# Kernel tuning notes

Measured on AMD Instinct MI355X. Metric: run time of the kernel, lower is better.

The kernel has to match this reference:

```python
import jax, jax.numpy as jnp
import numpy as np
from functools import partial

L, B, E, H, NL = 512, 16, 768, 12, 12
D = E // H  # head dim = 64
FF = 4 * E
LN_EPS = 1e-5


def gelu_new(x):
    # HF openai-gpt ACT_FNS['gelu'] (tanh approximation)
    c = np.sqrt(2.0 / np.pi).astype(np.float32)
    return 0.5 * x * (1.0 + jnp.tanh(c * (x + 0.044715 * x * x * x)))


def layer_norm(x, g, b):
    mu = jnp.mean(x, axis=-1, keepdims=True)
    var = jnp.mean(jnp.square(x - mu), axis=-1, keepdims=True)
    return (x - mu) * jax.lax.rsqrt(var + LN_EPS) * g + b


def setup_inputs() -> dict:
    key = jax.random.key(0)
    ks = jax.random.split(key, 8)
    s = 0.02
    x = jax.random.normal(ks[0], (L, B, E), dtype=jnp.float32)
    custom_mask = jnp.ones((B, L), dtype=jnp.float32)
    pos_emb = s * jax.random.normal(ks[1], (L, E), dtype=jnp.float32)
    # stacked per-layer params (leading axis = layer)
    params = {
        'c_attn_w': s * jax.random.normal(ks[2], (NL, E, 3 * E), dtype=jnp.float32),
        'c_attn_b': jnp.zeros((NL, 3 * E), dtype=jnp.float32),
        'attn_proj_w': s * jax.random.normal(ks[3], (NL, E, E), dtype=jnp.float32),
        'attn_proj_b': jnp.zeros((NL, E), dtype=jnp.float32),
        'ln1_g': jnp.ones((NL, E), dtype=jnp.float32),
        'ln1_b': jnp.zeros((NL, E), dtype=jnp.float32),
        'c_fc_w': s * jax.random.normal(ks[4], (NL, E, FF), dtype=jnp.float32),
        'c_fc_b': jnp.zeros((NL, FF), dtype=jnp.float32),
        'mlp_proj_w': s * jax.random.normal(ks[5], (NL, FF, E), dtype=jnp.float32),
        'mlp_proj_b': jnp.zeros((NL, E), dtype=jnp.float32),
        'ln2_g': jnp.ones((NL, E), dtype=jnp.float32),
        'ln2_b': jnp.zeros((NL, E), dtype=jnp.float32),
    }
    return {'x': x, 'custom_mask': custom_mask, 'pos_emb': pos_emb, **params}


def _gpt_forward(x, custom_mask, pos_emb, c_attn_w, c_attn_b, attn_proj_w,
                 attn_proj_b, ln1_g, ln1_b, c_fc_w, c_fc_b, mlp_proj_w,
                 mlp_proj_b, ln2_g, ln2_b):
    Lx, Bx, Ex = x.shape
    h = x.transpose(1, 0, 2) + pos_emb[None, :Lx]  # (B, L, E); dropout = eval identity
    # additive padding mask: (1 - m) * finfo.min, broadcast over heads/queries
    add_mask = (1.0 - custom_mask)[:, None, None, :] * jnp.finfo(jnp.float32).min
    causal = jnp.tril(jnp.ones((Lx, Lx), dtype=jnp.float32))  # bias buffer b

    def block(h, p):
        (caw, cab, apw, apb, g1, b1, fw, fb, pw, pb, g2, b2) = p
        qkv = h @ caw + cab                              # (B, L, 3E)
        q, k, v = jnp.split(qkv, 3, axis=-1)
        q = q.reshape(Bx, Lx, H, D).transpose(0, 2, 1, 3)  # (B, H, L, D)
        k = k.reshape(Bx, Lx, H, D).transpose(0, 2, 1, 3)
        v = v.reshape(Bx, Lx, H, D).transpose(0, 2, 1, 3)
        w = jnp.einsum('bhqd,bhkd->bhqk', q, k) / np.float32(np.sqrt(D))
        w = w * causal + (-10000.0) * (1.0 - causal)     # causal bias masking
        w = w + add_mask
        a = jax.nn.softmax(w, axis=-1)
        o = jnp.einsum('bhqk,bhkd->bhqd', a, v)          # (B, H, L, D)
        o = o.transpose(0, 2, 1, 3).reshape(Bx, Lx, Ex)
        a_out = o @ apw + apb
        n = layer_norm(h + a_out, g1, b1)
        m = gelu_new(n @ fw + fb) @ pw + pb
        h2 = layer_norm(n + m, g2, b2)
        return h2, None

    params = (c_attn_w, c_attn_b, attn_proj_w, attn_proj_b, ln1_g, ln1_b,
              c_fc_w, c_fc_b, mlp_proj_w, mlp_proj_b, ln2_g, ln2_b)
    h, _ = jax.lax.scan(block, h, params)
    return h.transpose(1, 0, 2)  # back to (L, B, E)


def reference(x, custom_mask, pos_emb, c_attn_w, c_attn_b, attn_proj_w,
              attn_proj_b, ln1_g, ln1_b, c_fc_w, c_fc_b, mlp_proj_w,
              mlp_proj_b, ln2_g, ln2_b):
    return _gpt_forward(x, custom_mask, pos_emb, c_attn_w, c_attn_b,
                        attn_proj_w, attn_proj_b, ln1_g, ln1_b, c_fc_w,
                        c_fc_b, mlp_proj_w, mlp_proj_b, ln2_g, ln2_b)
```

## Files before the change

kernel.cpp:

```cpp
#include <hip/hip_runtime.h>
#include <cstdint>
#include <cstddef>


#define LSEQ 512
#define NBATCH 16
#define EDIM 768
#define NHEAD 12
#define NLAYER 12

typedef __attribute__((ext_vector_type(8))) short short8;
typedef __attribute__((ext_vector_type(4))) float f32x4;

__device__ __forceinline__ short f2bf(float f) {
  union { float f; unsigned u; } x; x.f = f;
  return (short)((x.u + 0x7FFFu + ((x.u >> 16) & 1u)) >> 16);
}

__device__ __forceinline__ void gload_lds16(const void* g, void* l) {
  __builtin_amdgcn_global_load_lds(
      (__attribute__((address_space(1))) void*)(void*)g,
      (__attribute__((address_space(3))) void*)l, 16, 0, 0);
}

__global__ __launch_bounds__(256) void wt_transpose(const float* __restrict__ W,
                                                    short* __restrict__ Wt,
                                                    int K, int N) {
  __shared__ float tile[32][33];
  const int n0 = blockIdx.x * 32, k0 = blockIdx.y * 32;
  const size_t lo = (size_t)blockIdx.z * K * N;
  const float* Ws = W + lo;
  short* Wd = Wt + lo;
  const int tx = threadIdx.x & 31, ty = threadIdx.x >> 5;
#pragma unroll
  for (int i = 0; i < 4; ++i)
    tile[ty + i * 8][tx] = Ws[(size_t)(k0 + ty + i * 8) * N + n0 + tx];
  __syncthreads();
#pragma unroll
  for (int i = 0; i < 4; ++i)
    Wd[(size_t)(n0 + ty + i * 8) * K + k0 + tx] = f2bf(tile[tx][ty + i * 8]);
}

__global__ __launch_bounds__(256) void embed_k(const float* __restrict__ x,
                                               const float* __restrict__ pos,
                                               float* __restrict__ h,
                                               short* __restrict__ hbf) {
  const int row = blockIdx.x;
  const int b = row >> 9, lp = row & 511;
  const int t = threadIdx.x;
#pragma unroll
  for (int i = 0; i < 3; ++i) {
    const int e = t + i * 256;
    float v = x[(size_t)(lp * 16 + b) * 768 + e] + pos[(size_t)lp * 768 + e];
    h[(size_t)row * 768 + e] = v;
    hbf[(size_t)row * 768 + e] = f2bf(v);
  }
}

__global__ __launch_bounds__(256) void final_k(const float* __restrict__ h,
                                               float* __restrict__ out) {
  const int row = blockIdx.x;
  const int lp = row >> 4, b = row & 15;
  const int t = threadIdx.x;
#pragma unroll
  for (int i = 0; i < 3; ++i) {
    const int e = t + i * 256;
    out[(size_t)row * 768 + e] = h[(size_t)(b * 512 + lp) * 768 + e];
  }
}

__global__ __launch_bounds__(256) void ln_fused(const float* __restrict__ A,
                                                const float* __restrict__ B,
                                                const float* __restrict__ g,
                                                const float* __restrict__ be,
                                                float* __restrict__ outf,
                                                short* __restrict__ outb) {
  const int row = blockIdx.x;
  const int t = threadIdx.x;
  const size_t base = (size_t)row * 768;
  float v[3];
  float s1 = 0.f, s2 = 0.f;
#pragma unroll
  for (int i = 0; i < 3; ++i) {
    const int e = t + i * 256;
    float xv = A[base + e] + B[base + e];
    v[i] = xv; s1 += xv; s2 += xv * xv;
  }
#pragma unroll
  for (int m = 1; m < 64; m <<= 1) {
    s1 += __shfl_xor(s1, m);
    s2 += __shfl_xor(s2, m);
  }
  __shared__ float r1[4], r2[4];
  const int w = t >> 6, l = t & 63;
  if (l == 0) { r1[w] = s1; r2[w] = s2; }
  __syncthreads();
  s1 = r1[0] + r1[1] + r1[2] + r1[3];
  s2 = r2[0] + r2[1] + r2[2] + r2[3];
  const float mu = s1 * (1.f / 768.f);
  const float var = s2 * (1.f / 768.f) - mu * mu;
  const float rs = rsqrtf(var + 1e-5f);
#pragma unroll
  for (int i = 0; i < 3; ++i) {
    const int e = t + i * 256;
    float o = (v[i] - mu) * rs * g[e] + be[e];
    outf[base + e] = o;
    outb[base + e] = f2bf(o);
  }
}

template <int TN, int EPI>
__global__ __launch_bounds__(256) void gemm_bt(const short* __restrict__ A,
                                               const short* __restrict__ Bt,
                                               const float* __restrict__ bias,
                                               void* __restrict__ C,
                                               int N, int K) {
  constexpr int BK = 64;
  __shared__ alignas(16) short Alds[128 * BK];
  __shared__ alignas(16) short Blds[TN * BK];
  const int t = threadIdx.x;
  const int w = t >> 6, l = t & 63;
  constexpr int WR = (TN == 128) ? 2 : 4;
  constexpr int WC = (TN == 128) ? 2 : 1;
  constexpr int WM = 128 / WR;
  constexpr int MI = WM / 16;
  constexpr int NI = (TN / WC) / 16;
  const int wr = (WC == 2) ? (w >> 1) : w;
  const int wc = (WC == 2) ? (w & 1) : 0;
  const int l15 = l & 15, lhi = l >> 4;
  const int rowA0 = blockIdx.x * 128;
  const int rowB0 = blockIdx.y * TN;
  f32x4 acc[MI][NI];
#pragma unroll
  for (int mi = 0; mi < MI; ++mi)
#pragma unroll
    for (int ni = 0; ni < NI; ++ni) acc[mi][ni] = (f32x4){0.f, 0.f, 0.f, 0.f};

  const int srl = l >> 3;
  const int ss = l & 7;

  for (int kt = 0; kt < K; kt += BK) {
#pragma unroll
    for (int i = 0; i < 4; ++i) {
      const int r = i * 32 + w * 8 + srl;
      gload_lds16(A + (size_t)(rowA0 + r) * K + kt + ((ss ^ (r & 7)) << 3),
                  &Alds[i * 2048 + w * 512]);
    }
#pragma unroll
    for (int i = 0; i < TN / 32; ++i) {
      const int r = i * 32 + w * 8 + srl;
      gload_lds16(Bt + (size_t)(rowB0 + r) * K + kt + ((ss ^ (r & 7)) << 3),
                  &Blds[i * 2048 + w * 512]);
    }
    __syncthreads();
    short8 af[MI][2], bfr[NI][2];
#pragma unroll
    for (int mi = 0; mi < MI; ++mi) {
      const int r = wr * WM + mi * 16 + l15;
#pragma unroll
      for (int kc = 0; kc < 2; ++kc)
        af[mi][kc] = *(const short8*)
            &Alds[r * 64 + ((((kc << 2) | lhi) ^ (r & 7)) << 3)];
    }
#pragma unroll
    for (int ni = 0; ni < NI; ++ni) {
      const int r = wc * 64 + ni * 16 + l15;
#pragma unroll
      for (int kc = 0; kc < 2; ++kc)
        bfr[ni][kc] = *(const short8*)
            &Blds[r * 64 + ((((kc << 2) | lhi) ^ (r & 7)) << 3)];
    }
#pragma unroll
    for (int mi = 0; mi < MI; ++mi)
#pragma unroll
      for (int ni = 0; ni < NI; ++ni)
#pragma unroll
        for (int kc = 0; kc < 2; ++kc)
          acc[mi][ni] = __builtin_amdgcn_mfma_f32_16x16x32_bf16(
              af[mi][kc], bfr[ni][kc], acc[mi][ni], 0, 0, 0);
    __syncthreads();
  }

  float bv[NI];
#pragma unroll
  for (int ni = 0; ni < NI; ++ni) bv[ni] = bias[rowB0 + wc * 64 + ni * 16 + l15];
#pragma unroll
  for (int mi = 0; mi < MI; ++mi) {
#pragma unroll
    for (int ni = 0; ni < NI; ++ni) {
      const int col = rowB0 + wc * 64 + ni * 16 + l15;
#pragma unroll
      for (int i = 0; i < 4; ++i) {
        const int row = rowA0 + wr * WM + mi * 16 + lhi * 4 + i;
        float v = acc[mi][ni][i] + bv[ni];
        if constexpr (EPI == 0) {
          ((float*)C)[(size_t)row * N + col] = v;
        } else if constexpr (EPI == 1) {
          ((short*)C)[(size_t)row * N + col] = f2bf(v);
        } else {
          float z = 0.7978845608028654f * (v + 0.044715f * v * v * v);
          float th = 1.0f - 2.0f / (__expf(2.0f * z) + 1.0f);
          ((short*)C)[(size_t)row * N + col] = f2bf(0.5f * v * (1.0f + th));
        }
      }
    }
  }
}

__global__ __launch_bounds__(256) void attn_k(const short* __restrict__ qkv,
                                              const float* __restrict__ mask,
                                              short* __restrict__ o) {
  const int qb = blockIdx.x;
  const int hh = blockIdx.y;
  const int b = blockIdx.z;
  const int t = threadIdx.x, w = t >> 6, l = t & 63;
  const int l15 = l & 15, lhi = l >> 4;
  __shared__ alignas(16) short Klds[64 * 64];
  __shared__ alignas(16) short Vlds[64 * 64];
  __shared__ alignas(16) short Plds[4][16 * 72];

  short8 qa[2];
  {
    const size_t base =
        (size_t)(b * LSEQ + qb * 64 + w * 16 + l15) * 2304 + hh * 64;
    qa[0] = *(const short8*)&qkv[base + lhi * 8];
    qa[1] = *(const short8*)&qkv[base + 32 + lhi * 8];
  }
  float mrow[4] = {-1e30f, -1e30f, -1e30f, -1e30f};
  float lrow[4] = {0.f, 0.f, 0.f, 0.f};
  const f32x4 zero4 = {0.f, 0.f, 0.f, 0.f};
  f32x4 oacc[4];
#pragma unroll
  for (int nt = 0; nt < 4; ++nt) oacc[nt] = zero4;

  const int nkt = qb + 1;
  for (int kt = 0; kt < nkt; ++kt) {
    __syncthreads();
    {
      const int kr = t >> 2, cc = (t & 3) * 16;
      const size_t grow = (size_t)(b * LSEQ + kt * 64 + kr) * 2304 + hh * 64;
      short8 k0 = *(const short8*)&qkv[grow + 768 + cc];
      short8 k1 = *(const short8*)&qkv[grow + 768 + cc + 8];
      short8 v0 = *(const short8*)&qkv[grow + 1536 + cc];
      short8 v1 = *(const short8*)&qkv[grow + 1536 + cc + 8];
      const int sw = (kr & 7) << 4;
      *(short8*)((char*)Klds + ((kr * 128 + cc * 2) ^ sw)) = k0;
      *(short8*)((char*)Klds + ((kr * 128 + cc * 2 + 16) ^ sw)) = k1;
#pragma unroll
      for (int e = 0; e < 8; ++e) {
        const int n0 = cc + e, n1 = cc + 8 + e;
        ((short*)Vlds)[((n0 * 128 + kr * 2) ^ ((n0 & 7) << 4)) >> 1] = v0[e];
        ((short*)Vlds)[((n1 * 128 + kr * 2) ^ ((n1 & 7) << 4)) >> 1] = v1[e];
      }
    }
    __syncthreads();

    f32x4 s[4];
#pragma unroll
    for (int jt = 0; jt < 4; ++jt) {
      f32x4 z = zero4;
#pragma unroll
      for (int kc = 0; kc < 2; ++kc) {
        const int rowk = jt * 16 + l15;
        short8 kb = *(const short8*)((char*)Klds +
                     ((rowk * 128 + kc * 64 + lhi * 16) ^ ((rowk & 7) << 4)));
        z = __builtin_amdgcn_mfma_f32_16x16x32_bf16(qa[kc], kb, z, 0, 0, 0);
      }
      s[jt] = z;
    }

    float addm[4];
#pragma unroll
    for (int jt = 0; jt < 4; ++jt)
      addm[jt] = (1.0f - mask[b * LSEQ + kt * 64 + jt * 16 + l15]) *
                 -3.402823466e38f;
#pragma unroll
    for (int jt = 0; jt < 4; ++jt) {
      const int colg = kt * 64 + jt * 16 + l15;
#pragma unroll
      for (int i = 0; i < 4; ++i) {
        const int rowg = qb * 64 + w * 16 + lhi * 4 + i;
        float sv = s[jt][i] * 0.125f;
        if (colg > rowg) sv = -10000.0f;
        s[jt][i] = sv + addm[jt];
      }
    }

    float mnew[4], sc[4];
#pragma unroll
    for (int i = 0; i < 4; ++i) {
      float tm = fmaxf(fmaxf(s[0][i], s[1][i]), fmaxf(s[2][i], s[3][i]));
#pragma unroll
      for (int mm = 1; mm < 16; mm <<= 1) tm = fmaxf(tm, __shfl_xor(tm, mm));
      mnew[i] = fmaxf(mrow[i], tm);
      sc[i] = __expf(mrow[i] - mnew[i]);
      mrow[i] = mnew[i];
    }
#pragma unroll
    for (int i = 0; i < 4; ++i) {
      float ts = 0.f;
#pragma unroll
      for (int jt = 0; jt < 4; ++jt) {
        float p = __expf(s[jt][i] - mnew[i]);
        s[jt][i] = p;
        ts += p;
      }
#pragma unroll
      for (int mm = 1; mm < 16; mm <<= 1) ts += __shfl_xor(ts, mm);
      lrow[i] = lrow[i] * sc[i] + ts;
      oacc[0][i] *= sc[i]; oacc[1][i] *= sc[i];
      oacc[2][i] *= sc[i]; oacc[3][i] *= sc[i];
    }

    short* Pw = &Plds[w][0];
#pragma unroll
    for (int jt = 0; jt < 4; ++jt)
#pragma unroll
      for (int i = 0; i < 4; ++i)
        Pw[(lhi * 4 + i) * 72 + jt * 16 + l15] = f2bf(s[jt][i]);
    __syncthreads();
    short8 pa[2];
#pragma unroll
    for (int kc = 0; kc < 2; ++kc)
      pa[kc] = *(const short8*)&Pw[l15 * 72 + kc * 32 + lhi * 8];

#pragma unroll
    for (int nt = 0; nt < 4; ++nt) {
#pragma unroll
      for (int kc = 0; kc < 2; ++kc) {
        const int rown = nt * 16 + l15;
        short8 vb = *(const short8*)((char*)Vlds +
                     ((rown * 128 + kc * 64 + lhi * 16) ^ ((rown & 7) << 4)));
        oacc[nt] = __builtin_amdgcn_mfma_f32_16x16x32_bf16(pa[kc], vb,
                                                           oacc[nt], 0, 0, 0);
      }
    }
  }

#pragma unroll
  for (int i = 0; i < 4; ++i) {
    const size_t row = (size_t)(b * LSEQ + qb * 64 + w * 16 + lhi * 4 + i);
    const float inv = 1.0f / lrow[i];
#pragma unroll
    for (int nt = 0; nt < 4; ++nt)
      o[row * 768 + hh * 64 + nt * 16 + l15] = f2bf(oacc[nt][i] * inv);
  }
}

extern "C" void kernel_launch(void* const* d_in, const int* in_sizes, int n_in,
                              void* d_out, int out_size, void* d_ws,
                              size_t ws_size, hipStream_t stream) {
  const float* x    = (const float*)d_in[0];
  const float* mask = (const float*)d_in[1];
  const float* pos  = (const float*)d_in[2];
  const float* caw  = (const float*)d_in[3];
  const float* cab  = (const float*)d_in[4];
  const float* apw  = (const float*)d_in[5];
  const float* apb  = (const float*)d_in[6];
  const float* g1   = (const float*)d_in[7];
  const float* b1   = (const float*)d_in[8];
  const float* fw   = (const float*)d_in[9];
  const float* fb   = (const float*)d_in[10];
  const float* pw   = (const float*)d_in[11];
  const float* pb   = (const float*)d_in[12];
  const float* g2   = (const float*)d_in[13];
  const float* b2   = (const float*)d_in[14];

  char* ws = (char*)d_ws;
  size_t off = 0;
  auto alloc = [&](size_t bytes) {
    size_t o = off;
    off += (bytes + 255) & ~(size_t)255;
    return o;
  };
  float* h    = (float*)(ws + alloc(8192ull * 768 * 4));
  short* hbf  = (short*)(ws + alloc(8192ull * 768 * 2));
  float* nrm  = (float*)(ws + alloc(8192ull * 768 * 4));
  short* nbf  = (short*)(ws + alloc(8192ull * 768 * 2));
  short* qkvb = (short*)(ws + alloc(8192ull * 2304 * 2));
  short* obf  = (short*)(ws + alloc(8192ull * 768 * 2));
  float* aout = (float*)(ws + alloc(8192ull * 768 * 4));
  short* gbf  = (short*)(ws + alloc(8192ull * 3072 * 2));
  short* wt_attn = (short*)(ws + alloc(12ull * 768 * 2304 * 2));
  short* wt_proj = (short*)(ws + alloc(12ull * 768 * 768 * 2));
  short* wt_fc   = (short*)(ws + alloc(12ull * 768 * 3072 * 2));
  short* wt_mlp  = (short*)(ws + alloc(12ull * 3072 * 768 * 2));
  (void)ws_size; (void)in_sizes; (void)n_in; (void)out_size;

  wt_transpose<<<dim3(2304 / 32, 768 / 32, 12), 256, 0, stream>>>(caw, wt_attn, 768, 2304);
  wt_transpose<<<dim3(768 / 32, 768 / 32, 12), 256, 0, stream>>>(apw, wt_proj, 768, 768);
  wt_transpose<<<dim3(3072 / 32, 768 / 32, 12), 256, 0, stream>>>(fw, wt_fc, 768, 3072);
  wt_transpose<<<dim3(768 / 32, 3072 / 32, 12), 256, 0, stream>>>(pw, wt_mlp, 3072, 768);

  embed_k<<<8192, 256, 0, stream>>>(x, pos, h, hbf);

  for (int L = 0; L < 12; ++L) {
    gemm_bt<128, 1><<<dim3(64, 18), 256, 0, stream>>>(
        hbf, wt_attn + (size_t)L * 2304 * 768, cab + (size_t)L * 2304, qkvb, 2304, 768);
    attn_k<<<dim3(8, 12, 16), 256, 0, stream>>>(qkvb, mask, obf);
    gemm_bt<64, 0><<<dim3(64, 12), 256, 0, stream>>>(
        obf, wt_proj + (size_t)L * 768 * 768, apb + (size_t)L * 768, aout, 768, 768);
    ln_fused<<<8192, 256, 0, stream>>>(h, aout, g1 + (size_t)L * 768,
                                       b1 + (size_t)L * 768, nrm, nbf);
    gemm_bt<128, 2><<<dim3(64, 24), 256, 0, stream>>>(
        nbf, wt_fc + (size_t)L * 768 * 3072, fb + (size_t)L * 3072, gbf, 3072, 768);
    gemm_bt<64, 0><<<dim3(64, 12), 256, 0, stream>>>(
        gbf, wt_mlp + (size_t)L * 3072 * 768, pb + (size_t)L * 768, aout, 768, 3072);
    ln_fused<<<8192, 256, 0, stream>>>(nrm, aout, g2 + (size_t)L * 768,
                                       b2 + (size_t)L * 768, h, hbf);
  }

  final_k<<<8192, 256, 0, stream>>>(h, (float*)d_out);
}
```

Before: 3.372 ms.

## Double-buffer GEMM LDS tiles and simplify GELU epilogue to sigmoid form

The GEMM mainloop now keeps two LDS buffers for the A and B tiles. It issues the async global-to-LDS loads for the next K tile before running the MFMAs on the current one, so load latency can overlap with compute. It also precomputes per-thread source pointers and advances them each stage instead of recomputing addresses. The GELU epilogue is rewritten as x*sigmoid(1.5958*p) using a hardware reciprocal, which saves a division and some arithmetic. Doubling LDS per block may lower occupancy, and the reciprocal approximation slightly changes the numerics.

```diff
diff --git a/kernel.cpp b/kernel.cpp
--- a/kernel.cpp
+++ b/kernel.cpp
@@ -116,8 +116,8 @@
                                                void* __restrict__ C,
                                                int N, int K) {
   constexpr int BK = 64;
-  __shared__ alignas(16) short Alds[128 * BK];
-  __shared__ alignas(16) short Blds[TN * BK];
+  __shared__ alignas(16) short Alds[2][128 * BK];
+  __shared__ alignas(16) short Blds[2][TN * BK];
   const int t = threadIdx.x;
   const int w = t >> 6, l = t & 63;
   constexpr int WR = (TN == 128) ? 2 : 4;
@@ -139,20 +139,40 @@
   const int srl = l >> 3;
   const int ss = l & 7;
 
-  for (int kt = 0; kt < K; kt += BK) {
-#pragma unroll
-    for (int i = 0; i < 4; ++i) {
-      const int r = i * 32 + w * 8 + srl;
-      gload_lds16(A + (size_t)(rowA0 + r) * K + kt + ((ss ^ (r & 7)) << 3),
-                  &Alds[i * 2048 + w * 512]);
-    }
-#pragma unroll
-    for (int i = 0; i < TN / 32; ++i) {
-      const int r = i * 32 + w * 8 + srl;
-      gload_lds16(Bt + (size_t)(rowB0 + r) * K + kt + ((ss ^ (r & 7)) << 3),
-                  &Blds[i * 2048 + w * 512]);
-    }
-    __syncthreads();
+  const short* aptr[4];
+#pragma unroll
+  for (int i = 0; i < 4; ++i) {
+    const int r = i * 32 + w * 8 + srl;
+    aptr[i] = A + (size_t)(rowA0 + r) * K + ((ss ^ (r & 7)) << 3);
+  }
+  const short* bptr[TN / 32];
+#pragma unroll
+  for (int i = 0; i < TN / 32; ++i) {
+    const int r = i * 32 + w * 8 + srl;
+    bptr[i] = Bt + (size_t)(rowB0 + r) * K + ((ss ^ (r & 7)) << 3);
+  }
+
+  auto stage = [&](int buf) {
+#pragma unroll
+    for (int i = 0; i < 4; ++i)
+      gload_lds16(aptr[i], &Alds[buf][i * 2048 + w * 512]);
+#pragma unroll
+    for (int i = 0; i < TN / 32; ++i)
+      gload_lds16(bptr[i], &Blds[buf][i * 2048 + w * 512]);
+#pragma unroll
+    for (int i = 0; i < 4; ++i) aptr[i] += BK;
+#pragma unroll
+    for (int i = 0; i < TN / 32; ++i) bptr[i] += BK;
+  };
+
+  stage(0);
+  __syncthreads();
+
+  const int nk = K / BK;
+  for (int tt = 0; tt < nk; ++tt) {
+    const int cur = tt & 1;
+    if (tt + 1 < nk) stage(cur ^ 1);
+
     short8 af[MI][2], bfr[NI][2];
 #pragma unroll
     for (int mi = 0; mi < MI; ++mi) {
@@ -160,7 +180,7 @@
 #pragma unroll
       for (int kc = 0; kc < 2; ++kc)
         af[mi][kc] = *(const short8*)
-            &Alds[r * 64 + ((((kc << 2) | lhi) ^ (r & 7)) << 3)];
+            &Alds[cur][r * 64 + ((((kc << 2) | lhi) ^ (r & 7)) << 3)];
     }
 #pragma unroll
     for (int ni = 0; ni < NI; ++ni) {
@@ -168,7 +188,7 @@
 #pragma unroll
       for (int kc = 0; kc < 2; ++kc)
         bfr[ni][kc] = *(const short8*)
-            &Blds[r * 64 + ((((kc << 2) | lhi) ^ (r & 7)) << 3)];
+            &Blds[cur][r * 64 + ((((kc << 2) | lhi) ^ (r & 7)) << 3)];
     }
 #pragma unroll
     for (int mi = 0; mi < MI; ++mi)
@@ -198,9 +218,10 @@
         } else if constexpr (EPI == 1) {
           ((short*)C)[(size_t)row * N + col] = f2bf(v);
         } else {
-          float z = 0.7978845608028654f * (v + 0.044715f * v * v * v);
-          float th = 1.0f - 2.0f / (__expf(2.0f * z) + 1.0f);
-          ((short*)C)[(size_t)row * N + col] = f2bf(0.5f * v * (1.0f + th));
+          float p = v * fmaf(0.044715f, v * v, 1.0f);
+          float e = __expf(-1.5957691216057308f * p);
+          float r = __builtin_amdgcn_rcpf(1.0f + e);
+          ((short*)C)[(size_t)row * N + col] = f2bf(v * r);
         }
       }
     }
```

Result: slower. 3.485 ms (+3.4%).
